# Performance work log

Hardware: AMD Instinct MI355X
Metric: run time of the kernel (lower is better)

Reference implementation:

```python
import jax, jax.numpy as jnp
import numpy as np

B, T, N, D = 4, 12, 512, 128
L = 4            # max_lag + 1 lag encoders
H = D // 2       # lag-encoder hidden dim
THRESHOLD = 0.1


def setup_inputs() -> dict:
    key = jax.random.key(0)
    ks = jax.random.split(key, 10)
    s = 0.02
    return {
        "x":   jax.random.normal(ks[0], (B, T, N, D), dtype=jnp.float32),
        # lag encoders: Linear(D->H), ReLU, Linear(H->D), stacked over L lags
        "W1":  s * jax.random.normal(ks[1], (L, D, H), dtype=jnp.float32),
        "b1":  jnp.zeros((L, H), dtype=jnp.float32),
        "W2":  s * jax.random.normal(ks[2], (L, H, D), dtype=jnp.float32),
        "b2":  jnp.zeros((L, D), dtype=jnp.float32),
        # causal scorer: Linear(2D->D), ReLU, (Dropout=id in eval), Linear(D->1), Sigmoid
        "Ws1": s * jax.random.normal(ks[3], (2 * D, D), dtype=jnp.float32),
        "bs1": jnp.zeros((D,), dtype=jnp.float32),
        "Ws2": s * jax.random.normal(ks[4], (D, 1), dtype=jnp.float32),
        "bs2": jnp.zeros((1,), dtype=jnp.float32),
    }


def reference(x, W1, b1, W2, b2, Ws1, bs1, Ws2, bs2):
    Tdim = x.shape[1]
    # lagged slices x[:, T-1-lag] for lag in 0..L-1 (all lags active since T > max_lag)
    lags = jnp.stack([x[:, max(0, Tdim - 1 - l)] for l in range(L)], axis=1)  # (B,L,N,D)
    h = jax.nn.relu(jnp.einsum('blnd,ldh->blnh', lags, W1) + b1[None, :, None, :])
    enc = jnp.einsum('blnh,lhd->blnd', h, W2) + b2[None, :, None, :]          # (B,L,N,D)
    agg = enc.mean(axis=1)                                                    # (B,N,D)

    # pairwise causal scorer. cat([src, tgt]) @ Ws1 == src @ Ws1[:D] + tgt @ Ws1[D:],
    # avoiding the explicit (B,N,N,2D) concat.
    src_proj = jnp.einsum('bnd,dk->bnk', agg, Ws1[:D])   # (B,N,D)
    tgt_proj = jnp.einsum('bnd,dk->bnk', agg, Ws1[D:])   # (B,N,D)
    pre = src_proj[:, :, None, :] + tgt_proj[:, None, :, :] + bs1  # (B,N,N,D)
    score = jax.nn.sigmoid(jnp.einsum('bijd,d->bij', jax.nn.relu(pre), Ws2[:, 0]) + bs2[0])

    # threshold sparsification + remove self loops
    adj = jnp.where(score > THRESHOLD, score, 0.0)
    adj = adj * (1.0 - jnp.eye(N, dtype=adj.dtype))

    # multi-hop propagation and global max normalization per batch element
    a2 = jnp.matmul(adj, adj)
    a3 = jnp.matmul(a2, adj)
    enhanced = adj + 0.5 * a2 + 0.25 * a3
    mx = jnp.max(enhanced, axis=(-1, -2), keepdims=True)
    return enhanced / (mx + 1e-8)
```

## Files before the change

kernel.cpp:

```cpp
#include <hip/hip_runtime.h>
#include <math.h>

#define Bn 4
#define Tn 12
#define Nn 512
#define Dn 128
#define Ln 4
#define Hn 64

typedef __attribute__((ext_vector_type(8))) short short8;
typedef __attribute__((ext_vector_type(4))) float f32x4;
typedef _Float16 h2 __attribute__((ext_vector_type(2)));

__device__ __forceinline__ unsigned short f2bf(float f) {
    unsigned int u = __float_as_uint(f);
    unsigned int r = (u + 0x7FFF + ((u >> 16) & 1)) >> 16;
    return (unsigned short)r;
}
__device__ __forceinline__ float bf2f(unsigned short s) {
    return __uint_as_float(((unsigned int)s) << 16);
}
__device__ __forceinline__ float fdot2(h2 a, h2 b, float c) {
#if defined(__has_builtin)
#if __has_builtin(__builtin_amdgcn_fdot2)
    return __builtin_amdgcn_fdot2(a, b, c, false);
#else
    return c + (float)a.x*(float)b.x + (float)a.y*(float)b.y;
#endif
#else
    return c + (float)a.x*(float)b.x + (float)a.y*(float)b.y;
#endif
}

__global__ __launch_bounds__(256) void k_prep(
    const float* __restrict__ W1, const float* __restrict__ W2, const float* __restrict__ Ws1,
    unsigned short* __restrict__ w1p, unsigned short* __restrict__ w2p,
    unsigned short* __restrict__ wsp)
{
    int g = blockIdx.x*256 + threadIdx.x;
    unsigned short tmp[8];
    if (g < 4096) {
        int lag = g >> 10, r = g & 1023;
        int n = r >> 4, k8 = r & 15;
        #pragma unroll
        for (int j = 0; j < 8; ++j) tmp[j] = f2bf(W1[(size_t)(lag*128 + k8*8 + j)*64 + n]);
        *(short8*)(w1p + (size_t)lag*8192 + n*128 + k8*8) = *(const short8*)tmp;
    } else if (g < 8192) {
        int r = g - 4096;
        int n = r >> 5, k8 = r & 31;
        #pragma unroll
        for (int j = 0; j < 8; ++j) tmp[j] = f2bf(W2[(size_t)(k8*8 + j)*128 + n]);
        *(short8*)(w2p + (size_t)n*256 + k8*8) = *(const short8*)tmp;
    } else {
        int r = g - 8192;
        int tgt = r >> 11, r2 = r & 2047;
        int n = r2 >> 4, k8 = r2 & 15;
        #pragma unroll
        for (int j = 0; j < 8; ++j) tmp[j] = f2bf(Ws1[(size_t)(tgt*128 + k8*8 + j)*128 + n]);
        *(short8*)(wsp + (size_t)tgt*16384 + n*128 + k8*8) = *(const short8*)tmp;
    }
}

__global__ __launch_bounds__(512) void k_enc(
    const float* __restrict__ x,  const float* __restrict__ b1,
    const float* __restrict__ b2, const float* __restrict__ bs1,
    const unsigned short* __restrict__ w1p, const unsigned short* __restrict__ w2p,
    const unsigned short* __restrict__ wsp,
    unsigned short* __restrict__ spb, unsigned short* __restrict__ tpb,
    unsigned int* __restrict__ maxslot)
{
    __shared__ __align__(16) unsigned short xAll[4][16*136];
    __shared__ __align__(16) unsigned short hA[16*264];
    __shared__ __align__(16) unsigned short aggA[16*136];
    int tid  = threadIdx.x;
    int bid  = blockIdx.x;
    int wv   = __builtin_amdgcn_readfirstlane(tid >> 6);
    int lane = tid & 63;
    if (bid == 0 && tid < Bn) maxslot[tid] = 0u;

    int r0 = bid * 16;
    int bb = r0 >> 9, n0 = r0 & 511;
    int m = lane & 15, q = lane >> 4;
    int colL = lane & 15, rq = lane >> 4;

    for (int v = tid; v < 2048; v += 512) {
        int lag = v >> 9, r = v & 511;
        int row = r >> 5, c4 = r & 31;
        const float4* xs = (const float4*)(x + ((size_t)(bb*Tn + (Tn-1-lag))*Nn + n0)*Dn);
        float4 f = xs[row*32 + c4];
        ushort4 o = { f2bf(f.x), f2bf(f.y), f2bf(f.z), f2bf(f.w) };
        *(ushort4*)&xAll[lag][row*136 + c4*4] = o;
    }
    __syncthreads();

    {
        int lag = wv >> 1, hf = wv & 1;
        f32x4 acc[2] = {{0.f,0.f,0.f,0.f},{0.f,0.f,0.f,0.f}};
        #pragma unroll
        for (int ks = 0; ks < 4; ++ks) {
            short8 af = *(const short8*)&xAll[lag][m*136 + ks*32 + q*8];
            #pragma unroll
            for (int nt = 0; nt < 2; ++nt) {
                short8 bg = *(const short8*)(w1p + (size_t)lag*8192 + (hf*32 + nt*16 + m)*128 + ks*32 + q*8);
                acc[nt] = __builtin_amdgcn_mfma_f32_16x16x32_bf16(af, bg, acc[nt], 0, 0, 0);
            }
        }
        #pragma unroll
        for (int nt = 0; nt < 2; ++nt) {
            int ncol = hf*32 + nt*16 + colL;
            float bv = b1[lag*Hn + ncol];
            #pragma unroll
            for (int reg = 0; reg < 4; ++reg)
                hA[(rq*4+reg)*264 + lag*64 + ncol] = f2bf(fmaxf(acc[nt][reg] + bv, 0.f));
        }
    }
    __syncthreads();

    {
        f32x4 acc = {0.f,0.f,0.f,0.f};
        #pragma unroll
        for (int ks = 0; ks < 8; ++ks) {
            short8 af = *(const short8*)&hA[m*264 + ks*32 + q*8];
            short8 bg = *(const short8*)(w2p + (size_t)(wv*16 + m)*256 + ks*32 + q*8);
            acc = __builtin_amdgcn_mfma_f32_16x16x32_bf16(af, bg, acc, 0, 0, 0);
        }
        int col = wv*16 + colL;
        float b2s = b2[col] + b2[Dn+col] + b2[2*Dn+col] + b2[3*Dn+col];
        #pragma unroll
        for (int reg = 0; reg < 4; ++reg)
            aggA[(rq*4+reg)*136 + col] = f2bf(0.25f*(acc[reg] + b2s));
    }
    __syncthreads();

    {
        int tgt = wv >> 2, wv4 = wv & 3;
        f32x4 acc[2] = {{0.f,0.f,0.f,0.f},{0.f,0.f,0.f,0.f}};
        #pragma unroll
        for (int ks = 0; ks < 4; ++ks) {
            short8 af = *(const short8*)&aggA[m*136 + ks*32 + q*8];
            #pragma unroll
            for (int nt = 0; nt < 2; ++nt) {
                short8 bg = *(const short8*)(wsp + (size_t)tgt*16384 + (wv4*32 + nt*16 + m)*128 + ks*32 + q*8);
                acc[nt] = __builtin_amdgcn_mfma_f32_16x16x32_bf16(af, bg, acc[nt], 0, 0, 0);
            }
        }
        unsigned short* dst = tgt ? tpb : spb;
        #pragma unroll
        for (int nt = 0; nt < 2; ++nt) {
            int n = wv4*32 + nt*16 + colL;
            float bv = tgt ? 0.f : bs1[n];
            #pragma unroll
            for (int reg = 0; reg < 4; ++reg) {
                _Float16 hv = (_Float16)(acc[nt][reg] + bv);
                dst[(size_t)(r0 + rq*4 + reg)*Dn + n] = __builtin_bit_cast(unsigned short, hv);
            }
        }
    }
}

__global__ __launch_bounds__(256) void k_score(
    const unsigned short* __restrict__ spb, const unsigned short* __restrict__ tpb,
    const float* __restrict__ Ws2, const float* __restrict__ bs2,
    unsigned short* __restrict__ adj_b, unsigned short* __restrict__ adj_bt)
{
    __shared__ unsigned int spl[64*65];
    __shared__ unsigned int tpl[64*65];
    __shared__ unsigned int wl[64];
    int tid = threadIdx.x;
    int wv = __builtin_amdgcn_readfirstlane(tid >> 6);
    int lane = tid & 63;
    int bz = blockIdx.z;
    int i0b = blockIdx.y * 64, j0b = blockIdx.x * 64;
    const unsigned short* spr = spb + (size_t)bz*Nn*Dn;
    const unsigned short* tpr = tpb + (size_t)bz*Nn*Dn;

    for (int v = tid; v < 1024; v += 256) {
        int row = v >> 4, c = v & 15;
        uint4 gs = *(const uint4*)(spr + (size_t)(i0b+row)*Dn + c*8);
        uint4 gt = *(const uint4*)(tpr + (size_t)(j0b+row)*Dn + c*8);
        spl[row*65 + c*4 + 0] = gs.x; spl[row*65 + c*4 + 1] = gs.y;
        spl[row*65 + c*4 + 2] = gs.z; spl[row*65 + c*4 + 3] = gs.w;
        tpl[row*65 + c*4 + 0] = gt.x; tpl[row*65 + c*4 + 1] = gt.y;
        tpl[row*65 + c*4 + 2] = gt.z; tpl[row*65 + c*4 + 3] = gt.w;
    }
    if (tid < 64) {
        h2 hw = { (_Float16)Ws2[tid*2], (_Float16)Ws2[tid*2+1] };
        wl[tid] = __builtin_bit_cast(unsigned int, hw);
    }
    __syncthreads();

    int iq = lane >> 4, jq = lane & 15;
    int iw = wv*16 + iq*4;
    float acc[4][4] = {};
    #pragma unroll 4
    for (int c = 0; c < 64; ++c) {
        h2 wp = __builtin_bit_cast(h2, wl[c]);
        h2 sh[4], th[4];
        #pragma unroll
        for (int ii = 0; ii < 4; ++ii) sh[ii] = __builtin_bit_cast(h2, spl[(iw+ii)*65 + c]);
        #pragma unroll
        for (int jj = 0; jj < 4; ++jj) th[jj] = __builtin_bit_cast(h2, tpl[(jq*4+jj)*65 + c]);
        #pragma unroll
        for (int ii = 0; ii < 4; ++ii)
            #pragma unroll
            for (int jj = 0; jj < 4; ++jj) {
                h2 r = __builtin_elementwise_max(sh[ii] + th[jj], (h2){(_Float16)0.f,(_Float16)0.f});
                acc[ii][jj] = fdot2(r, wp, acc[ii][jj]);
            }
    }
    float bsv = bs2[0];
    int i0 = i0b + iw;
    int j0 = j0b + jq*4;
    float vals[4][4];
    #pragma unroll
    for (int ii = 0; ii < 4; ++ii) {
        int i = i0 + ii;
        #pragma unroll
        for (int jj = 0; jj < 4; ++jj) {
            float z = acc[ii][jj] + bsv;
            float sc = 1.f/(1.f + __expf(-z));
            int j = j0 + jj;
            vals[ii][jj] = (sc > 0.1f && i != j) ? sc : 0.f;
        }
    }
    size_t base = (size_t)bz << 18;
    #pragma unroll
    for (int ii = 0; ii < 4; ++ii) {
        ushort4 rv = make_ushort4(f2bf(vals[ii][0]), f2bf(vals[ii][1]),
                                  f2bf(vals[ii][2]), f2bf(vals[ii][3]));
        *(ushort4*)(adj_b + base + (size_t)(i0+ii)*Nn + j0) = rv;
    }
    #pragma unroll
    for (int jj = 0; jj < 4; ++jj) {
        ushort4 cv = make_ushort4(f2bf(vals[0][jj]), f2bf(vals[1][jj]),
                                  f2bf(vals[2][jj]), f2bf(vals[3][jj]));
        *(ushort4*)(adj_bt + base + (size_t)(j0+jj)*Nn + i0) = cv;
    }
}

__global__ __launch_bounds__(256) void k_mm1(
    const unsigned short* __restrict__ adj_b, const unsigned short* __restrict__ adj_bt,
    unsigned short* __restrict__ a2b)
{
    __shared__ unsigned short Als[64*72];
    __shared__ unsigned short Bls[64*72];
    int tid = threadIdx.x;
    int wv = __builtin_amdgcn_readfirstlane(tid >> 6);
    int lane = tid & 63;
    int b = blockIdx.z, i0 = blockIdx.y*64, j0 = blockIdx.x*64;
    size_t base = (size_t)b << 18;
    const unsigned short* Ab = adj_b + base;
    const unsigned short* Bb = adj_bt + base;
    int wm = wv >> 1, wn = wv & 1;
    int m = lane & 15, q = lane >> 4;
    int sr = tid >> 2, sc = (tid & 3)*16;
    f32x4 acc[2][2];
    #pragma unroll
    for (int mt = 0; mt < 2; ++mt)
        #pragma unroll
        for (int nt = 0; nt < 2; ++nt) acc[mt][nt] = (f32x4){0.f,0.f,0.f,0.f};
    short8 pa0, pa1, pb0, pb1;
    pa0 = *(const short8*)(Ab + (size_t)(i0+sr)*Nn + sc);
    pa1 = *(const short8*)(Ab + (size_t)(i0+sr)*Nn + sc + 8);
    pb0 = *(const short8*)(Bb + (size_t)(j0+sr)*Nn + sc);
    pb1 = *(const short8*)(Bb + (size_t)(j0+sr)*Nn + sc + 8);
    for (int kt = 0; kt < 8; ++kt) {
        *(short8*)&Als[sr*72 + sc]     = pa0;
        *(short8*)&Als[sr*72 + sc + 8] = pa1;
        *(short8*)&Bls[sr*72 + sc]     = pb0;
        *(short8*)&Bls[sr*72 + sc + 8] = pb1;
        __syncthreads();
        if (kt < 7) {
            int k0 = (kt+1)*64;
            pa0 = *(const short8*)(Ab + (size_t)(i0+sr)*Nn + k0 + sc);
            pa1 = *(const short8*)(Ab + (size_t)(i0+sr)*Nn + k0 + sc + 8);
            pb0 = *(const short8*)(Bb + (size_t)(j0+sr)*Nn + k0 + sc);
            pb1 = *(const short8*)(Bb + (size_t)(j0+sr)*Nn + k0 + sc + 8);
        }
        #pragma unroll
        for (int ks = 0; ks < 2; ++ks) {
            short8 af[2], bg[2];
            #pragma unroll
            for (int mt = 0; mt < 2; ++mt) af[mt] = *(const short8*)&Als[(wm*32+mt*16+m)*72 + ks*32 + q*8];
            #pragma unroll
            for (int nt = 0; nt < 2; ++nt) bg[nt] = *(const short8*)&Bls[(wn*32+nt*16+m)*72 + ks*32 + q*8];
            #pragma unroll
            for (int mt = 0; mt < 2; ++mt)
                #pragma unroll
                for (int nt = 0; nt < 2; ++nt)
                    acc[mt][nt] = __builtin_amdgcn_mfma_f32_16x16x32_bf16(af[mt], bg[nt], acc[mt][nt], 0, 0, 0);
        }
        __syncthreads();
    }
    int col = lane & 15, rq = lane >> 4;
    #pragma unroll
    for (int mt = 0; mt < 2; ++mt)
        #pragma unroll
        for (int nt = 0; nt < 2; ++nt)
            #pragma unroll
            for (int reg = 0; reg < 4; ++reg) {
                int i = i0 + wm*32 + mt*16 + rq*4 + reg;
                int j = j0 + wn*32 + nt*16 + col;
                a2b[base + (size_t)i*Nn + j] = f2bf(acc[mt][nt][reg]);
            }
}

__global__ __launch_bounds__(256) void k_mm2(
    const unsigned short* __restrict__ adj_b, const unsigned short* __restrict__ adj_bt,
    const unsigned short* __restrict__ a2b,
    float* __restrict__ out, unsigned int* __restrict__ maxslot)
{
    __shared__ unsigned short Als[64*72];
    __shared__ unsigned short Bls[64*72];
    __shared__ float red[4];
    int tid = threadIdx.x;
    int wv = __builtin_amdgcn_readfirstlane(tid >> 6);
    int lane = tid & 63;
    int b = blockIdx.z, i0 = blockIdx.y*64, j0 = blockIdx.x*64;
    size_t base = (size_t)b << 18;
    const unsigned short* Ab = a2b + base;
    const unsigned short* Bb = adj_bt + base;
    int wm = wv >> 1, wn = wv & 1;
    int m = lane & 15, q = lane >> 4;
    int sr = tid >> 2, sc = (tid & 3)*16;
    f32x4 acc[2][2];
    #pragma unroll
    for (int mt = 0; mt < 2; ++mt)
        #pragma unroll
        for (int nt = 0; nt < 2; ++nt) acc[mt][nt] = (f32x4){0.f,0.f,0.f,0.f};
    short8 pa0, pa1, pb0, pb1;
    pa0 = *(const short8*)(Ab + (size_t)(i0+sr)*Nn + sc);
    pa1 = *(const short8*)(Ab + (size_t)(i0+sr)*Nn + sc + 8);
    pb0 = *(const short8*)(Bb + (size_t)(j0+sr)*Nn + sc);
    pb1 = *(const short8*)(Bb + (size_t)(j0+sr)*Nn + sc + 8);
    for (int kt = 0; kt < 8; ++kt) {
        *(short8*)&Als[sr*72 + sc]     = pa0;
        *(short8*)&Als[sr*72 + sc + 8] = pa1;
        *(short8*)&Bls[sr*72 + sc]     = pb0;
        *(short8*)&Bls[sr*72 + sc + 8] = pb1;
        __syncthreads();
        if (kt < 7) {
            int k0 = (kt+1)*64;
            pa0 = *(const short8*)(Ab + (size_t)(i0+sr)*Nn + k0 + sc);
            pa1 = *(const short8*)(Ab + (size_t)(i0+sr)*Nn + k0 + sc + 8);
            pb0 = *(const short8*)(Bb + (size_t)(j0+sr)*Nn + k0 + sc);
            pb1 = *(const short8*)(Bb + (size_t)(j0+sr)*Nn + k0 + sc + 8);
        }
        #pragma unroll
        for (int ks = 0; ks < 2; ++ks) {
            short8 af[2], bg[2];
            #pragma unroll
            for (int mt = 0; mt < 2; ++mt) af[mt] = *(const short8*)&Als[(wm*32+mt*16+m)*72 + ks*32 + q*8];
            #pragma unroll
            for (int nt = 0; nt < 2; ++nt) bg[nt] = *(const short8*)&Bls[(wn*32+nt*16+m)*72 + ks*32 + q*8];
            #pragma unroll
            for (int mt = 0; mt < 2; ++mt)
                #pragma unroll
                for (int nt = 0; nt < 2; ++nt)
                    acc[mt][nt] = __builtin_amdgcn_mfma_f32_16x16x32_bf16(af[mt], bg[nt], acc[mt][nt], 0, 0, 0);
        }
        __syncthreads();
    }
    int col = lane & 15, rq = lane >> 4;
    float lmax = 0.f;
    const unsigned short* adjp = adj_b + base;
    #pragma unroll
    for (int mt = 0; mt < 2; ++mt)
        #pragma unroll
        for (int nt = 0; nt < 2; ++nt)
            #pragma unroll
            for (int reg = 0; reg < 4; ++reg) {
                int i = i0 + wm*32 + mt*16 + rq*4 + reg;
                int j = j0 + wn*32 + nt*16 + col;
                size_t off = (size_t)i*Nn + j;
                float e = bf2f(adjp[off]) + 0.5f*bf2f(Ab[off]) + 0.25f*acc[mt][nt][reg];
                out[base + off] = e;
                lmax = fmaxf(lmax, e);
            }
    #pragma unroll
    for (int s = 1; s < 64; s <<= 1) lmax = fmaxf(lmax, __shfl_xor(lmax, s, 64));
    if (lane == 0) red[wv] = lmax;
    __syncthreads();
    if (tid == 0) {
        float mx = fmaxf(fmaxf(red[0], red[1]), fmaxf(red[2], red[3]));
        atomicMax(maxslot + b, __float_as_uint(mx));
    }
}

__global__ __launch_bounds__(256) void k_norm(float* __restrict__ out,
                                              const unsigned int* __restrict__ maxslot)
{
    int idx = blockIdx.x*256 + threadIdx.x;
    int b = idx >> 16;
    float m = __uint_as_float(maxslot[b]);
    float inv = 1.f/(m + 1e-8f);
    float4* p = (float4*)out + idx;
    float4 v = *p;
    v.x *= inv; v.y *= inv; v.z *= inv; v.w *= inv;
    *p = v;
}

extern "C" void kernel_launch(void* const* d_in, const int* in_sizes, int n_in,
                              void* d_out, int out_size, void* d_ws, size_t ws_size,
                              hipStream_t stream) {
    const float* x   = (const float*)d_in[0];
    const float* W1  = (const float*)d_in[1];
    const float* b1  = (const float*)d_in[2];
    const float* W2  = (const float*)d_in[3];
    const float* b2  = (const float*)d_in[4];
    const float* Ws1 = (const float*)d_in[5];
    const float* bs1 = (const float*)d_in[6];
    const float* Ws2 = (const float*)d_in[7];
    const float* bs2 = (const float*)d_in[8];
    float* out = (float*)d_out;

    unsigned char* wsb = (unsigned char*)d_ws;
    unsigned short* spb    = (unsigned short*)(wsb);
    unsigned short* tpb    = (unsigned short*)(wsb + (512u<<10));
    unsigned short* adj_b  = (unsigned short*)(wsb + (1024u<<10));
    unsigned short* adj_bt = (unsigned short*)(wsb + (3072u<<10));
    unsigned short* a2b    = (unsigned short*)(wsb + (5120u<<10));
    unsigned int*   maxslot= (unsigned int*)(wsb + (7168u<<10));
    unsigned short* w1p    = (unsigned short*)(wsb + (7172u<<10));
    unsigned short* w2p    = (unsigned short*)(wsb + (7236u<<10));
    unsigned short* wsp    = (unsigned short*)(wsb + (7300u<<10));

    k_prep <<<dim3(48),       256, 0, stream>>>(W1, W2, Ws1, w1p, w2p, wsp);
    k_enc  <<<dim3(128),      512, 0, stream>>>(x, b1, b2, bs1, w1p, w2p, wsp, spb, tpb, maxslot);
    k_score<<<dim3(8, 8, Bn), 256, 0, stream>>>(spb, tpb, Ws2, bs2, adj_b, adj_bt);
    k_mm1  <<<dim3(8, 8, Bn), 256, 0, stream>>>(adj_b, adj_bt, a2b);
    k_mm2  <<<dim3(8, 8, Bn), 256, 0, stream>>>(adj_b, adj_bt, a2b, out, maxslot);
    k_norm <<<dim3(1024),     256, 0, stream>>>(out, maxslot);
}
```

Baseline: 117.1 us.

## Pre-pack transposed adjacency in MFMA fragment layout and double-buffer A tiles

The score kernel now writes the transposed adjacency in a layout that matches the MFMA B-operand fragments. Each lane of the two matmul kernels can then load its B fragment with one coalesced 16-byte global load straight into registers, with no LDS staging. The A tile moves to a double-buffered LDS scheme with one barrier per k-step instead of two. B fragments are register-prefetched two steps ahead, which raises register pressure and relies on the packed-index arithmetic being correct.

```diff
diff --git a/kernel.cpp b/kernel.cpp
--- a/kernel.cpp
+++ b/kernel.cpp
@@ -161,7 +161,7 @@
 __global__ __launch_bounds__(256) void k_score(
     const unsigned short* __restrict__ spb, const unsigned short* __restrict__ tpb,
     const float* __restrict__ Ws2, const float* __restrict__ bs2,
-    unsigned short* __restrict__ adj_b, unsigned short* __restrict__ adj_bt)
+    unsigned short* __restrict__ adj_b, unsigned short* __restrict__ adj_pk)
 {
     __shared__ unsigned int spl[64*65];
     __shared__ unsigned int tpl[64*65];
@@ -230,67 +230,87 @@
                                   f2bf(vals[ii][2]), f2bf(vals[ii][3]));
         *(ushort4*)(adj_b + base + (size_t)(i0+ii)*Nn + j0) = rv;
     }
+    int kblk = i0 >> 5, qq = (i0 >> 3) & 3, t0 = i0 & 7;
     #pragma unroll
     for (int jj = 0; jj < 4; ++jj) {
+        int j = j0 + jj;
+        int jt = j >> 4, mm = j & 15;
         ushort4 cv = make_ushort4(f2bf(vals[0][jj]), f2bf(vals[1][jj]),
                                   f2bf(vals[2][jj]), f2bf(vals[3][jj]));
-        *(ushort4*)(adj_bt + base + (size_t)(j0+jj)*Nn + i0) = cv;
+        *(ushort4*)(adj_pk + base + (size_t)(kblk*32 + jt)*512 + (qq*16 + mm)*8 + t0) = cv;
     }
 }
 
 __global__ __launch_bounds__(256) void k_mm1(
-    const unsigned short* __restrict__ adj_b, const unsigned short* __restrict__ adj_bt,
+    const unsigned short* __restrict__ adj_b, const unsigned short* __restrict__ adj_pk,
     unsigned short* __restrict__ a2b)
 {
-    __shared__ unsigned short Als[64*72];
-    __shared__ unsigned short Bls[64*72];
+    __shared__ unsigned short Als[2][64*72];
     int tid = threadIdx.x;
     int wv = __builtin_amdgcn_readfirstlane(tid >> 6);
     int lane = tid & 63;
     int b = blockIdx.z, i0 = blockIdx.y*64, j0 = blockIdx.x*64;
     size_t base = (size_t)b << 18;
     const unsigned short* Ab = adj_b + base;
-    const unsigned short* Bb = adj_bt + base;
+    const unsigned short* pkB = adj_pk + base + (size_t)lane*8;
     int wm = wv >> 1, wn = wv & 1;
     int m = lane & 15, q = lane >> 4;
     int sr = tid >> 2, sc = (tid & 3)*16;
+    int jtb = (j0 >> 4) + wn*2;
     f32x4 acc[2][2];
     #pragma unroll
     for (int mt = 0; mt < 2; ++mt)
         #pragma unroll
         for (int nt = 0; nt < 2; ++nt) acc[mt][nt] = (f32x4){0.f,0.f,0.f,0.f};
-    short8 pa0, pa1, pb0, pb1;
-    pa0 = *(const short8*)(Ab + (size_t)(i0+sr)*Nn + sc);
-    pa1 = *(const short8*)(Ab + (size_t)(i0+sr)*Nn + sc + 8);
-    pb0 = *(const short8*)(Bb + (size_t)(j0+sr)*Nn + sc);
-    pb1 = *(const short8*)(Bb + (size_t)(j0+sr)*Nn + sc + 8);
+
+    *(short8*)&Als[0][sr*72 + sc]     = *(const short8*)(Ab + (size_t)(i0+sr)*Nn + sc);
+    *(short8*)&Als[0][sr*72 + sc + 8] = *(const short8*)(Ab + (size_t)(i0+sr)*Nn + sc + 8);
+    short8 pa0 = *(const short8*)(Ab + (size_t)(i0+sr)*Nn + 64 + sc);
+    short8 pa1 = *(const short8*)(Ab + (size_t)(i0+sr)*Nn + 64 + sc + 8);
+    short8 bfr[2][2][2];
+    #pragma unroll
+    for (int p = 0; p < 2; ++p)
+        #pragma unroll
+        for (int ks = 0; ks < 2; ++ks)
+            #pragma unroll
+            for (int nt = 0; nt < 2; ++nt)
+                bfr[p][ks][nt] = *(const short8*)(pkB + (size_t)((p*2+ks)*32 + jtb + nt)*512);
+
+    #pragma unroll
     for (int kt = 0; kt < 8; ++kt) {
-        *(short8*)&Als[sr*72 + sc]     = pa0;
-        *(short8*)&Als[sr*72 + sc + 8] = pa1;
-        *(short8*)&Bls[sr*72 + sc]     = pb0;
-        *(short8*)&Bls[sr*72 + sc + 8] = pb1;
         __syncthreads();
         if (kt < 7) {
-            int k0 = (kt+1)*64;
-            pa0 = *(const short8*)(Ab + (size_t)(i0+sr)*Nn + k0 + sc);
-            pa1 = *(const short8*)(Ab + (size_t)(i0+sr)*Nn + k0 + sc + 8);
-            pb0 = *(const short8*)(Bb + (size_t)(j0+sr)*Nn + k0 + sc);
-            pb1 = *(const short8*)(Bb + (size_t)(j0+sr)*Nn + k0 + sc + 8);
+            *(short8*)&Als[(kt+1)&1][sr*72 + sc]     = pa0;
+            *(short8*)&Als[(kt+1)&1][sr*72 + sc + 8] = pa1;
+        }
+        if (kt < 6) {
+            pa0 = *(const short8*)(Ab + (size_t)(i0+sr)*Nn + (kt+2)*64 + sc);
+            pa1 = *(const short8*)(Ab + (size_t)(i0+sr)*Nn + (kt+2)*64 + sc + 8);
+        }
+        short8 cur[2][2];
+        #pragma unroll
+        for (int ks = 0; ks < 2; ++ks)
+            #pragma unroll
+            for (int nt = 0; nt < 2; ++nt) cur[ks][nt] = bfr[kt&1][ks][nt];
+        if (kt < 6) {
+            #pragma unroll
+            for (int ks = 0; ks < 2; ++ks)
+                #pragma unroll
+                for (int nt = 0; nt < 2; ++nt)
+                    bfr[kt&1][ks][nt] = *(const short8*)(pkB + (size_t)(((kt+2)*2+ks)*32 + jtb + nt)*512);
         }
         #pragma unroll
         for (int ks = 0; ks < 2; ++ks) {
-            short8 af[2], bg[2];
-            #pragma unroll
-            for (int mt = 0; mt < 2; ++mt) af[mt] = *(const short8*)&Als[(wm*32+mt*16+m)*72 + ks*32 + q*8];
-            #pragma unroll
-            for (int nt = 0; nt < 2; ++nt) bg[nt] = *(const short8*)&Bls[(wn*32+nt*16+m)*72 + ks*32 + q*8];
+            short8 af[2];
+            #pragma unroll
+            for (int mt = 0; mt < 2; ++mt)
+                af[mt] = *(const short8*)&Als[kt&1][(wm*32+mt*16+m)*72 + ks*32 + q*8];
             #pragma unroll
             for (int mt = 0; mt < 2; ++mt)
                 #pragma unroll
                 for (int nt = 0; nt < 2; ++nt)
-                    acc[mt][nt] = __builtin_amdgcn_mfma_f32_16x16x32_bf16(af[mt], bg[nt], acc[mt][nt], 0, 0, 0);
-        }
-        __syncthreads();
+                    acc[mt][nt] = __builtin_amdgcn_mfma_f32_16x16x32_bf16(af[mt], cur[ks][nt], acc[mt][nt], 0, 0, 0);
+        }
     }
     int col = lane & 15, rq = lane >> 4;
     #pragma unroll
@@ -306,12 +326,11 @@
 }
 
 __global__ __launch_bounds__(256) void k_mm2(
-    const unsigned short* __restrict__ adj_b, const unsigned short* __restrict__ adj_bt,
+    const unsigned short* __restrict__ adj_b, const unsigned short* __restrict__ adj_pk,
     const unsigned short* __restrict__ a2b,
     float* __restrict__ out, unsigned int* __restrict__ maxslot)
 {
-    __shared__ unsigned short Als[64*72];
-    __shared__ unsigned short Bls[64*72];
+    __shared__ unsigned short Als[2][64*72];
     __shared__ float red[4];
     int tid = threadIdx.x;
     int wv = __builtin_amdgcn_readfirstlane(tid >> 6);
@@ -319,47 +338,65 @@
     int b = blockIdx.z, i0 = blockIdx.y*64, j0 = blockIdx.x*64;
     size_t base = (size_t)b << 18;
     const unsigned short* Ab = a2b + base;
-    const unsigned short* Bb = adj_bt + base;
+    const unsigned short* pkB = adj_pk + base + (size_t)lane*8;
     int wm = wv >> 1, wn = wv & 1;
     int m = lane & 15, q = lane >> 4;
     int sr = tid >> 2, sc = (tid & 3)*16;
+    int jtb = (j0 >> 4) + wn*2;
     f32x4 acc[2][2];
     #pragma unroll
     for (int mt = 0; mt < 2; ++mt)
         #pragma unroll
         for (int nt = 0; nt < 2; ++nt) acc[mt][nt] = (f32x4){0.f,0.f,0.f,0.f};
-    short8 pa0, pa1, pb0, pb1;
-    pa0 = *(const short8*)(Ab + (size_t)(i0+sr)*Nn + sc);
-    pa1 = *(const short8*)(Ab + (size_t)(i0+sr)*Nn + sc + 8);
-    pb0 = *(const short8*)(Bb + (size_t)(j0+sr)*Nn + sc);
-    pb1 = *(const short8*)(Bb + (size_t)(j0+sr)*Nn + sc + 8);
+
+    *(short8*)&Als[0][sr*72 + sc]     = *(const short8*)(Ab + (size_t)(i0+sr)*Nn + sc);
+    *(short8*)&Als[0][sr*72 + sc + 8] = *(const short8*)(Ab + (size_t)(i0+sr)*Nn + sc + 8);
+    short8 pa0 = *(const short8*)(Ab + (size_t)(i0+sr)*Nn + 64 + sc);
+    short8 pa1 = *(const short8*)(Ab + (size_t)(i0+sr)*Nn + 64 + sc + 8);
+    short8 bfr[2][2][2];
+    #pragma unroll
+    for (int p = 0; p < 2; ++p)
+        #pragma unroll
+        for (int ks = 0; ks < 2; ++ks)
+            #pragma unroll
+            for (int nt = 0; nt < 2; ++nt)
+                bfr[p][ks][nt] = *(const short8*)(pkB + (size_t)((p*2+ks)*32 + jtb + nt)*512);
+
+    #pragma unroll
     for (int kt = 0; kt < 8; ++kt) {
-        *(short8*)&Als[sr*72 + sc]     = pa0;
-        *(short8*)&Als[sr*72 + sc + 8] = pa1;
-        *(short8*)&Bls[sr*72 + sc]     = pb0;
-        *(short8*)&Bls[sr*72 + sc + 8] = pb1;
         __syncthreads();
         if (kt < 7) {
-            int k0 = (kt+1)*64;
-            pa0 = *(const short8*)(Ab + (size_t)(i0+sr)*Nn + k0 + sc);
-            pa1 = *(const short8*)(Ab + (size_t)(i0+sr)*Nn + k0 + sc + 8);
-            pb0 = *(const short8*)(Bb + (size_t)(j0+sr)*Nn + k0 + sc);
-            pb1 = *(const short8*)(Bb + (size_t)(j0+sr)*Nn + k0 + sc + 8);
+            *(short8*)&Als[(kt+1)&1][sr*72 + sc]     = pa0;
+            *(short8*)&Als[(kt+1)&1][sr*72 + sc + 8] = pa1;
+        }
+        if (kt < 6) {
+            pa0 = *(const short8*)(Ab + (size_t)(i0+sr)*Nn + (kt+2)*64 + sc);
+            pa1 = *(const short8*)(Ab + (size_t)(i0+sr)*Nn + (kt+2)*64 + sc + 8);
+        }
+        short8 cur[2][2];
+        #pragma unroll
+        for (int ks = 0; ks < 2; ++ks)
+            #pragma unroll
+            for (int nt = 0; nt < 2; ++nt) cur[ks][nt] = bfr[kt&1][ks][nt];
+        if (kt < 6) {
+            #pragma unroll
+            for (int ks = 0; ks < 2; ++ks)
+                #pragma unroll
+                for (int nt = 0; nt < 2; ++nt)
+                    bfr[kt&1][ks][nt] = *(const short8*)(pkB + (size_t)(((kt+2)*2+ks)*32 + jtb + nt)*512);
         }
         #pragma unroll
         for (int ks = 0; ks < 2; ++ks) {
-            short8 af[2], bg[2];
-            #pragma unroll
-            for (int mt = 0; mt < 2; ++mt) af[mt] = *(const short8*)&Als[(wm*32+mt*16+m)*72 + ks*32 + q*8];
-            #pragma unroll
-            for (int nt = 0; nt < 2; ++nt) bg[nt] = *(const short8*)&Bls[(wn*32+nt*16+m)*72 + ks*32 + q*8];
+            short8 af[2];
+            #pragma unroll
+            for (int mt = 0; mt < 2; ++mt)
+                af[mt] = *(const short8*)&Als[kt&1][(wm*32+mt*16+m)*72 + ks*32 + q*8];
             #pragma unroll
             for (int mt = 0; mt < 2; ++mt)
                 #pragma unroll
                 for (int nt = 0; nt < 2; ++nt)
-                    acc[mt][nt] = __builtin_amdgcn_mfma_f32_16x16x32_bf16(af[mt], bg[nt], acc[mt][nt], 0, 0, 0);
-        }
-        __syncthreads();
+                    acc[mt][nt] = __builtin_amdgcn_mfma_f32_16x16x32_bf16(af[mt], cur[ks][nt], acc[mt][nt], 0, 0, 0);
+        }
     }
     int col = lane & 15, rq = lane >> 4;
     float lmax = 0.f;
@@ -418,7 +455,7 @@
     unsigned short* spb    = (unsigned short*)(wsb);
     unsigned short* tpb    = (unsigned short*)(wsb + (512u<<10));
     unsigned short* adj_b  = (unsigned short*)(wsb + (1024u<<10));
-    unsigned short* adj_bt = (unsigned short*)(wsb + (3072u<<10));
+    unsigned short* adj_pk = (unsigned short*)(wsb + (3072u<<10));
     unsigned short* a2b    = (unsigned short*)(wsb + (5120u<<10));
     unsigned int*   maxslot= (unsigned int*)(wsb + (7168u<<10));
     unsigned short* w1p    = (unsigned short*)(wsb + (7172u<<10));
@@ -427,8 +464,8 @@
 
     k_prep <<<dim3(48),       256, 0, stream>>>(W1, W2, Ws1, w1p, w2p, wsp);
     k_enc  <<<dim3(128),      512, 0, stream>>>(x, b1, b2, bs1, w1p, w2p, wsp, spb, tpb, maxslot);
-    k_score<<<dim3(8, 8, Bn), 256, 0, stream>>>(spb, tpb, Ws2, bs2, adj_b, adj_bt);
-    k_mm1  <<<dim3(8, 8, Bn), 256, 0, stream>>>(adj_b, adj_bt, a2b);
-    k_mm2  <<<dim3(8, 8, Bn), 256, 0, stream>>>(adj_b, adj_bt, a2b, out, maxslot);
+    k_score<<<dim3(8, 8, Bn), 256, 0, stream>>>(spb, tpb, Ws2, bs2, adj_b, adj_pk);
+    k_mm1  <<<dim3(8, 8, Bn), 256, 0, stream>>>(adj_b, adj_pk, a2b);
+    k_mm2  <<<dim3(8, 8, Bn), 256, 0, stream>>>(adj_b, adj_pk, a2b, out, maxslot);
     k_norm <<<dim3(1024),     256, 0, stream>>>(out, maxslot);
 }
```

New measurement: 112.6 us. 3.9% less time.
